# Kernel tuning notes

Measured on AMD Instinct MI355X. Metric: run time of the kernel, lower is better.

The kernel has to match this reference:

```python
import jax, jax.numpy as jnp
import numpy as np

GROUPS = 32
EPS = 1e-6


def group_norm(x, scale, bias):
    b, c, h, w = x.shape
    xg = x.reshape(b, GROUPS, c // GROUPS, h, w)
    mean = xg.mean(axis=(2, 3, 4), keepdims=True)
    var = xg.var(axis=(2, 3, 4), keepdims=True)
    xg = (xg - mean) * jax.lax.rsqrt(var + EPS)
    x = xg.reshape(b, c, h, w)
    return x * scale[None, :, None, None] + bias[None, :, None, None]


def conv1x1(x, w, b):
    # x: [B,C,H,W], w: [O,C], b: [O]
    return jnp.einsum('bchw,oc->bohw', x, w) + b[None, :, None, None]


def setup_inputs() -> dict:
    key = jax.random.key(0)
    ks = jax.random.split(key, 11)
    B, C, H, W = 4, 512, 64, 64
    s = 1.0 / np.sqrt(C)
    return {
        'x': jax.random.normal(ks[0], (B, C, H, W), jnp.float32),
        'gn_scale': jnp.ones((C,), jnp.float32),
        'gn_bias': jnp.zeros((C,), jnp.float32),
        'wq': jax.random.normal(ks[1], (C, C), jnp.float32) * s,
        'bq': jnp.zeros((C,), jnp.float32),
        'wk': jax.random.normal(ks[2], (C, C), jnp.float32) * s,
        'bk': jnp.zeros((C,), jnp.float32),
        'wv': jax.random.normal(ks[3], (C, C), jnp.float32) * s,
        'bv': jnp.zeros((C,), jnp.float32),
        'wp': jax.random.normal(ks[4], (C, C), jnp.float32) * s,
        'bp': jnp.zeros((C,), jnp.float32),
    }


def reference(x, gn_scale, gn_bias, wq, bq, wk, bk, wv, bv, wp, bp):
    b, c, h, w = x.shape
    h_ = group_norm(x, gn_scale, gn_bias)
    q = conv1x1(h_, wq, bq).reshape(b, c, h * w)  # [B,C,N]
    k = conv1x1(h_, wk, bk).reshape(b, c, h * w)
    v = conv1x1(h_, wv, bv).reshape(b, c, h * w)
    # scores[b,i,j] = sum_c q[b,c,i]*k[b,c,j] / sqrt(c)
    scores = jnp.einsum('bci,bcj->bij', q, k) * (c ** -0.5)
    attn = jax.nn.softmax(scores, axis=2)
    # out[b,c,i] = sum_j attn[b,i,j] * v[b,c,j]
    out = jnp.einsum('bij,bcj->bci', attn, v).reshape(b, c, h, w)
    out = conv1x1(out, wp, bp)
    return x + out
```

## Files before the change

kernel.cpp:

```cpp
#include <hip/hip_runtime.h>

#define CDIM 512
#define NDIM 4096
#define BATCH 4

using bf8v = __attribute__((ext_vector_type(8))) __bf16;
using f4v  = __attribute__((ext_vector_type(4))) float;

typedef __attribute__((address_space(1))) unsigned int gu32;
typedef __attribute__((address_space(3))) unsigned int lu32;

static __device__ __forceinline__ unsigned short f2bf(float f) {
  unsigned int u = __float_as_uint(f);
  u += 0x7fffu + ((u >> 16) & 1u);
  return (unsigned short)(u >> 16);
}

static __device__ __forceinline__ bf8v lds_read16(const unsigned short* p) {
  bf8v r;
  unsigned off = (unsigned)(unsigned long long)p;
  asm volatile("ds_read_b128 %0, %1" : "=v"(r) : "v"(off));
  return r;
}

__global__ __launch_bounds__(256) void gn_stats_kernel(
    const float* __restrict__ x, float* __restrict__ stats) {
  const int tid = threadIdx.x;
  const float4* xv = (const float4*)(x + (long)blockIdx.x * 65536);
  float s = 0.f, ss = 0.f;
  for (int i = tid; i < 16384; i += 256) {
    float4 d = xv[i];
    s  += d.x + d.y + d.z + d.w;
    ss += d.x * d.x + d.y * d.y + d.z * d.z + d.w * d.w;
  }
#pragma unroll
  for (int off = 32; off; off >>= 1) {
    s  += __shfl_down(s, off);
    ss += __shfl_down(ss, off);
  }
  __shared__ float red[8];
  if ((tid & 63) == 0) { red[tid >> 6] = s; red[4 + (tid >> 6)] = ss; }
  __syncthreads();
  if (tid == 0) {
    float S  = red[0] + red[1] + red[2] + red[3];
    float SS = red[4] + red[5] + red[6] + red[7];
    float mean = S * (1.f / 65536.f);
    float var  = SS * (1.f / 65536.f) - mean * mean;
    stats[blockIdx.x * 2]     = mean;
    stats[blockIdx.x * 2 + 1] = rsqrtf(var + 1e-6f);
  }
}

__global__ __launch_bounds__(256) void gn_transpose_kernel(
    const float* __restrict__ x, const float* __restrict__ gs,
    const float* __restrict__ gb, const float* __restrict__ stats,
    unsigned short* __restrict__ hT) {
  __shared__ float t[64][65];
  const int tid = threadIdx.x;
  const int b = blockIdx.z;
  const long bbx = (long)b * ((long)CDIM * NDIM);
  const int n0 = blockIdx.x * 64, c0 = blockIdx.y * 64;
  for (int k = 0; k < 4; ++k) {
    int it = tid + k * 256;
    int c = it >> 4, no = (it & 15) << 2;
    int ch = c0 + c;
    int g = ch >> 4;
    float mean = stats[(b * 32 + g) * 2];
    float rstd = stats[(b * 32 + g) * 2 + 1];
    float a  = rstd * gs[ch];
    float bb = gb[ch] - mean * a;
    float4 d = *(const float4*)&x[bbx + (long)ch * NDIM + n0 + no];
    t[no + 0][c] = d.x * a + bb;
    t[no + 1][c] = d.y * a + bb;
    t[no + 2][c] = d.z * a + bb;
    t[no + 3][c] = d.w * a + bb;
  }
  __syncthreads();
  const long bbh = (long)b * ((long)NDIM * CDIM);
  for (int k = 0; k < 2; ++k) {
    int it = tid + k * 256;
    int n = it >> 3, co = (it & 7) << 3;
    unsigned int ow[4];
#pragma unroll
    for (int j = 0; j < 4; ++j) {
      unsigned short lo = f2bf(t[n][co + 2 * j]);
      unsigned short hi = f2bf(t[n][co + 2 * j + 1]);
      ow[j] = (unsigned int)lo | ((unsigned int)hi << 16);
    }
    uint4 o; o.x = ow[0]; o.y = ow[1]; o.z = ow[2]; o.w = ow[3];
    *(uint4*)&hT[bbh + (long)(n0 + n) * CDIM + c0 + co] = o;
  }
}

__global__ __launch_bounds__(256) void prep_kernel(
    const float* __restrict__ wq, const float* __restrict__ wk,
    const float* __restrict__ wv, const float* __restrict__ bq,
    const float* __restrict__ bk, unsigned short* __restrict__ wqkb,
    unsigned short* __restrict__ wvb, float* __restrict__ bqk) {
  int blk = blockIdx.x;
  if (blk < 768) {
    int i = blk * 256 + threadIdx.x;
    const float* src = (blk < 256) ? wq : (blk < 512) ? wk : wv;
    unsigned short* dst = (blk < 256) ? wqkb : (blk < 512) ? (wqkb + 262144) : wvb;
    int j = i - ((blk < 256) ? 0 : (blk < 512) ? 65536 : 131072);
    float4 d = ((const float4*)src)[j];
    ushort4 o;
    o.x = f2bf(d.x); o.y = f2bf(d.y); o.z = f2bf(d.z); o.w = f2bf(d.w);
    ((ushort4*)dst)[j] = o;
  } else {
#pragma unroll
    for (int k = 0; k < 4; ++k) {
      int i = threadIdx.x + k * 256;
      bqk[i] = (i < 512) ? bq[i] : bk[i - 512];
    }
  }
}

__global__ __launch_bounds__(256) void cvt_kernel(
    const float* __restrict__ src, unsigned short* __restrict__ dst, int n4) {
  int i = blockIdx.x * 256 + threadIdx.x;
  if (i >= n4) return;
  float4 d = ((const float4*)src)[i];
  ushort4 o;
  o.x = f2bf(d.x); o.y = f2bf(d.y); o.z = f2bf(d.z); o.w = f2bf(d.w);
  ((ushort4*)dst)[i] = o;
}

template <int BM, int BN, int EPI, int ORD>
__global__ __launch_bounds__(512, 2) void gemm8(
    const unsigned short* __restrict__ A, long sA, int lA,
    const unsigned short* __restrict__ B, long sB, int lB,
    void* __restrict__ Cp, long sC,
    const float* __restrict__ bias,
    const float* __restrict__ X, long sX,
    int GX, int GY, int Nn, int K) {
  constexpr int TM = BM / 32;
  constexpr int TN = BN / 64;
  constexpr int LA = BM / 128;
  constexpr int LB = BN / 128;
  constexpr int VN = 2 * (LA + LB);

  __shared__ __align__(16) unsigned short As[4 * BM * 32];
  __shared__ __align__(16) unsigned short Bs[4 * BN * 32];

  const int tid = threadIdx.x;
  const int nwg = gridDim.x;
  const int g = (blockIdx.x & 7) * (nwg >> 3) + (blockIdx.x >> 3);
  int bx, by, bz;
  if (ORD == 0) { bx = g % GX; int t = g / GX; by = t % GY; bz = t / GY; }
  else          { by = g % GY; int t = g / GY; bx = t % GX; bz = t / GX; }

  A += (long)bz * sA;
  B += (long)bz * sB;
  const int m0 = by * BM;
  const int n0 = bx * BN;
  const int lane = tid & 63;
  const int wv = tid >> 6;
  const int wm = (wv >> 2) * (BM / 2);
  const int wn = (wv & 3) * (BN / 4);
  const int l16 = lane & 15;
  const int quad = lane >> 4;
  const int rdo = ((quad ^ ((l16 >> 1) & 3)) << 3);

  const int rl = tid >> 2;
  const int gl = tid & 3;
  const int swl = ((gl ^ ((rl >> 1) & 3)) << 3);
  const unsigned short* Ag = A + (long)(m0 + rl) * lA + swl;
  const unsigned short* Bg = B + (long)(n0 + rl) * lB + swl;
  unsigned short* Asl = As + wv * 512;
  unsigned short* Bsl = Bs + wv * 512;

  const int nchunk = K >> 5;

  auto stageA = [&](int c) {
    if (c < nchunk) {
#pragma unroll
      for (int i = 0; i < LA; ++i)
        __builtin_amdgcn_global_load_lds(
            (const gu32*)(Ag + (long)i * 128 * lA + c * 32),
            (lu32*)(Asl + (c & 3) * (BM * 32) + i * 4096), 16, 0, 0);
    }
  };
  auto stageB = [&](int c) {
    if (c < nchunk) {
#pragma unroll
      for (int i = 0; i < LB; ++i)
        __builtin_amdgcn_global_load_lds(
            (const gu32*)(Bg + (long)i * 128 * lB + c * 32),
            (lu32*)(Bsl + (c & 3) * (BN * 32) + i * 4096), 16, 0, 0);
    }
  };

  f4v acc[TM][TN] = {};
  f4v accr[TM] = {};
  bf8v ones;
#pragma unroll
  for (int i = 0; i < 8; ++i) ones[i] = (__bf16)1.0f;

  auto body = [&](int d) {
    __builtin_amdgcn_s_barrier();
    stageA(d + 3);
    stageB(d + 3);
    const unsigned short* Ab = As + (d & 3) * (BM * 32);
    const unsigned short* Bb = Bs + (d & 3) * (BN * 32);
    bf8v af[TM], bf[TN];
#pragma unroll
    for (int t = 0; t < TM; ++t)
      af[t] = lds_read16(&Ab[(wm + t * 16 + l16) * 32 + rdo]);
#pragma unroll
    for (int t = 0; t < TN; ++t)
      bf[t] = lds_read16(&Bb[(wn + t * 16 + l16) * 32 + rdo]);
    asm volatile("s_waitcnt lgkmcnt(0)");
    __builtin_amdgcn_sched_barrier(0);
    __builtin_amdgcn_s_setprio(1);
#pragma unroll
    for (int tm = 0; tm < TM; ++tm) {
#pragma unroll
      for (int tn = 0; tn < TN; ++tn)
        acc[tm][tn] = __builtin_amdgcn_mfma_f32_16x16x32_bf16(
            af[tm], bf[tn], acc[tm][tn], 0, 0, 0);
      if (EPI == 3)
        accr[tm] = __builtin_amdgcn_mfma_f32_16x16x32_bf16(
            af[tm], ones, accr[tm], 0, 0, 0);
    }
    __builtin_amdgcn_s_setprio(0);
  };

  stageA(0); stageB(0); stageA(1); stageB(1); stageA(2); stageB(2);

  int d = 0;
  for (; d < nchunk - 2; ++d) {
    if constexpr (VN == 8) asm volatile("s_waitcnt vmcnt(8)");
    else                   asm volatile("s_waitcnt vmcnt(6)");
    body(d);
  }
  if constexpr (VN == 8) asm volatile("s_waitcnt vmcnt(4)");
  else                   asm volatile("s_waitcnt vmcnt(3)");
  body(d); ++d;
  asm volatile("s_waitcnt vmcnt(0)");
  body(d);

  if (EPI == 2) {
#pragma unroll
    for (int tm = 0; tm < TM; ++tm) {
#pragma unroll
      for (int r = 0; r < 4; ++r) {
        const int row = m0 + wm + tm * 16 + quad * 4 + r;
#pragma unroll
        for (int tn = 0; tn < TN; ++tn) {
          const int col = n0 + wn + tn * 16 + l16;
          float e = __expf(acc[tm][tn][r] * 0.044194173824159216f);
          ((unsigned short*)Cp)[(long)bz * sC + (long)row * Nn + col] = f2bf(e);
        }
      }
    }
  } else if (EPI == 3) {
#pragma unroll
    for (int tm = 0; tm < TM; ++tm) {
#pragma unroll
      for (int r = 0; r < 4; ++r) {
        const int row = m0 + wm + tm * 16 + quad * 4 + r;
        const float inv = 1.0f / accr[tm][r];
#pragma unroll
        for (int tn = 0; tn < TN; ++tn) {
          const int col = n0 + wn + tn * 16 + l16;
          ((unsigned short*)Cp)[(long)bz * sC + (long)row * Nn + col] =
              f2bf(acc[tm][tn][r] * inv);
        }
      }
    }
  } else {
#pragma unroll
    for (int tm = 0; tm < TM; ++tm) {
#pragma unroll
      for (int tn = 0; tn < TN; ++tn) {
        const int col = n0 + wn + tn * 16 + l16;
#pragma unroll
        for (int r = 0; r < 4; ++r) {
          const int row = m0 + wm + tm * 16 + quad * 4 + r;
          float val = acc[tm][tn][r];
          if (EPI == 0) {
            val += bias[col];
            ((unsigned short*)Cp)[(long)bz * sC + (long)row * Nn + col] = f2bf(val);
          } else if (EPI == 1) {
            val += bias[row];
            ((unsigned short*)Cp)[(long)bz * sC + (long)row * Nn + col] = f2bf(val);
          } else {
            ((float*)Cp)[(long)bz * sC + (long)row * Nn + col] =
                val + bias[row] + X[(long)bz * sX + (long)row * Nn + col];
          }
        }
      }
    }
  }
}

extern "C" void kernel_launch(void* const* d_in, const int* in_sizes, int n_in,
                              void* d_out, int out_size, void* d_ws, size_t ws_size,
                              hipStream_t stream) {
  (void)in_sizes; (void)n_in; (void)out_size;
  const float* x  = (const float*)d_in[0];
  const float* gs = (const float*)d_in[1];
  const float* gb = (const float*)d_in[2];
  const float* wq = (const float*)d_in[3];
  const float* bq = (const float*)d_in[4];
  const float* wk = (const float*)d_in[5];
  const float* bk = (const float*)d_in[6];
  const float* wv = (const float*)d_in[7];
  const float* bv = (const float*)d_in[8];
  const float* wp = (const float*)d_in[9];
  const float* bp = (const float*)d_in[10];
  float* out = (float*)d_out;

  char* ws = (char*)d_ws;
  const long NC  = (long)NDIM * CDIM;
  const long NQK = (long)NDIM * 1024;
  const long BUF = NC * 2 * BATCH;
  const long NN  = (long)NDIM * NDIM;

  unsigned short* hT   = (unsigned short*)(ws);
  unsigned short* OT   = hT;
  unsigned short* qkT  = (unsigned short*)(ws + BUF);
  unsigned short* vB   = (unsigned short*)(ws + BUF * 3);
  unsigned short* sc   = (unsigned short*)(ws + BUF * 4);
  unsigned short* wqkb = sc;
  unsigned short* wvb  = (unsigned short*)(ws + BUF * 4 + 1048576);
  float* bqk           = (float*)(ws + BUF * 4 + 1572864);
  float* stats         = (float*)(ws + BUF * 4 + 1581056);
  unsigned short* wpb  = qkT;

  gn_stats_kernel<<<BATCH * 32, 256, 0, stream>>>(x, stats);
  gn_transpose_kernel<<<dim3(NDIM / 64, CDIM / 64, BATCH), 256, 0, stream>>>(x, gs, gb, stats, hT);
  prep_kernel<<<769, 256, 0, stream>>>(wq, wk, wv, bq, bk, wqkb, wvb, bqk);

  gemm8<256, 256, 0, 0><<<256, 512, 0, stream>>>(
      hT, NC, CDIM, wqkb, 0, CDIM, qkT, NQK, bqk, nullptr, 0, 4, 16, 1024, CDIM);
  gemm8<128, 256, 1, 1><<<256, 512, 0, stream>>>(
      wvb, 0, CDIM, hT, NC, CDIM, vB, NC, bv, nullptr, 0, 16, 4, NDIM, CDIM);

  if (ws_size >= (size_t)(BUF * 4) + (size_t)(NN * 2) * BATCH) {
    gemm8<256, 256, 2, 0><<<1024, 512, 0, stream>>>(
        qkT, NQK, 1024, qkT + 512, NQK, 1024, sc, NN, nullptr, nullptr, 0,
        16, 16, NDIM, CDIM);
    gemm8<128, 256, 3, 1><<<256, 512, 0, stream>>>(
        sc, NN, NDIM, vB, NC, NDIM, OT, NC, nullptr, nullptr, 0,
        2, 32, CDIM, NDIM);
  } else {
    for (int b = 0; b < BATCH; ++b) {
      gemm8<256, 256, 2, 0><<<256, 512, 0, stream>>>(
          qkT + b * NQK, 0, 1024, qkT + b * NQK + 512, 0, 1024, sc, 0,
          nullptr, nullptr, 0, 16, 16, NDIM, CDIM);
      gemm8<128, 256, 3, 1><<<64, 512, 0, stream>>>(
          sc, 0, NDIM, vB + b * NC, 0, NDIM, OT + b * NC, 0,
          nullptr, nullptr, 0, 2, 32, CDIM, NDIM);
    }
  }

  cvt_kernel<<<256, 256, 0, stream>>>(wp, wpb, 65536);
  gemm8<128, 256, 4, 1><<<256, 512, 0, stream>>>(
      wpb, 0, CDIM, OT, NC, CDIM, out, NC, bp, x, NC, 16, 4, NDIM, CDIM);
}
```

Before: 358.5 us.

## Double-buffer LDS fragment reads to overlap with MFMA in GEMM main loop

Restructures the GEMM K-loop so the LDS fragment reads for the next chunk are issued before the MFMAs of the current chunk run, using two register fragment sets (A/B ping-pong) and a loop unrolled by two. The aim is to hide LDS read latency behind matrix math instead of waiting on lgkmcnt before each chunk's MFMAs. It also merges the A/B staging lambdas and retunes the vmcnt waits. In exchange it doubles the fragment registers, which may pressure occupancy under launch_bounds(512,2). The pipeline tail assumes an even chunk count.

```diff
diff --git a/kernel.cpp b/kernel.cpp
--- a/kernel.cpp
+++ b/kernel.cpp
@@ -138,7 +138,7 @@
   constexpr int TN = BN / 64;
   constexpr int LA = BM / 128;
   constexpr int LB = BN / 128;
-  constexpr int VN = 2 * (LA + LB);
+  constexpr int L  = LA + LB;
 
   __shared__ __align__(16) unsigned short As[4 * BM * 32];
   __shared__ __align__(16) unsigned short Bs[4 * BN * 32];
@@ -172,17 +172,13 @@
 
   const int nchunk = K >> 5;
 
-  auto stageA = [&](int c) {
+  auto stage = [&](int c) {
     if (c < nchunk) {
 #pragma unroll
       for (int i = 0; i < LA; ++i)
         __builtin_amdgcn_global_load_lds(
             (const gu32*)(Ag + (long)i * 128 * lA + c * 32),
             (lu32*)(Asl + (c & 3) * (BM * 32) + i * 4096), 16, 0, 0);
-    }
-  };
-  auto stageB = [&](int c) {
-    if (c < nchunk) {
 #pragma unroll
       for (int i = 0; i < LB; ++i)
         __builtin_amdgcn_global_load_lds(
@@ -197,21 +193,20 @@
 #pragma unroll
   for (int i = 0; i < 8; ++i) ones[i] = (__bf16)1.0f;
 
-  auto body = [&](int d) {
-    __builtin_amdgcn_s_barrier();
-    stageA(d + 3);
-    stageB(d + 3);
-    const unsigned short* Ab = As + (d & 3) * (BM * 32);
-    const unsigned short* Bb = Bs + (d & 3) * (BN * 32);
-    bf8v af[TM], bf[TN];
+  bf8v afA[TM], bfA[TN], afB[TM], bfB[TN];
+
+  auto readfr = [&](int c, bf8v* af, bf8v* bf) {
+    const unsigned short* Ab = As + (c & 3) * (BM * 32);
+    const unsigned short* Bb = Bs + (c & 3) * (BN * 32);
 #pragma unroll
     for (int t = 0; t < TM; ++t)
       af[t] = lds_read16(&Ab[(wm + t * 16 + l16) * 32 + rdo]);
 #pragma unroll
     for (int t = 0; t < TN; ++t)
       bf[t] = lds_read16(&Bb[(wn + t * 16 + l16) * 32 + rdo]);
-    asm volatile("s_waitcnt lgkmcnt(0)");
-    __builtin_amdgcn_sched_barrier(0);
+  };
+
+  auto mfma = [&](const bf8v* af, const bf8v* bf) {
     __builtin_amdgcn_s_setprio(1);
 #pragma unroll
     for (int tm = 0; tm < TM; ++tm) {
@@ -226,19 +221,37 @@
     __builtin_amdgcn_s_setprio(0);
   };
 
-  stageA(0); stageB(0); stageA(1); stageB(1); stageA(2); stageB(2);
+  auto seg = [&](int d, const bf8v* afC, const bf8v* bfC,
+                 bf8v* afN, bf8v* bfN) {
+    __builtin_amdgcn_s_barrier();
+    stage(d + 3);
+    asm volatile("s_waitcnt lgkmcnt(0)");
+    __builtin_amdgcn_sched_barrier(0);
+    readfr(d + 1, afN, bfN);
+    __builtin_amdgcn_sched_barrier(0);
+    mfma(afC, bfC);
+  };
+
+  stage(0); stage(1); stage(2);
+  if constexpr (L == 4) asm volatile("s_waitcnt vmcnt(8)");
+  else                  asm volatile("s_waitcnt vmcnt(6)");
+  __builtin_amdgcn_s_barrier();
+  readfr(0, afA, bfA);
 
   int d = 0;
-  for (; d < nchunk - 2; ++d) {
-    if constexpr (VN == 8) asm volatile("s_waitcnt vmcnt(8)");
-    else                   asm volatile("s_waitcnt vmcnt(6)");
-    body(d);
-  }
-  if constexpr (VN == 8) asm volatile("s_waitcnt vmcnt(4)");
-  else                   asm volatile("s_waitcnt vmcnt(3)");
-  body(d); ++d;
+  for (; d < nchunk - 2; d += 2) {
+    if constexpr (L == 4) asm volatile("s_waitcnt vmcnt(4)");
+    else                  asm volatile("s_waitcnt vmcnt(3)");
+    seg(d, afA, bfA, afB, bfB);
+    if constexpr (L == 4) asm volatile("s_waitcnt vmcnt(4)");
+    else                  asm volatile("s_waitcnt vmcnt(3)");
+    seg(d + 1, afB, bfB, afA, bfA);
+  }
   asm volatile("s_waitcnt vmcnt(0)");
-  body(d);
+  seg(d, afA, bfA, afB, bfB);
+  asm volatile("s_waitcnt lgkmcnt(0)");
+  __builtin_amdgcn_sched_barrier(0);
+  mfma(afB, bfB);
 
   if (EPI == 2) {
 #pragma unroll
```

New measurement: 363.0 us. Within noise of the previous version (+1.3%).

## Switch GEMM mainloop to K=64 double-buffered tiles with interleaved LDS reads and MFMA

Applied to the files above, without the earlier changes.

Restructures the bf16 GEMM mainloop from a 4-stage ring of K=32 chunks to a 2-stage double buffer of K=64 tiles with a new XOR swizzle. Within each tile, A-fragment LDS reads are split into clusters and issued ahead of the MFMA groups, with partial lgkmcnt waits, so LDS latency overlaps compute. This halves the number of barriers per K. The cost is shallower global prefetch: each iteration now does a full vmcnt(0) wait, which may expose global-load latency.

```diff
diff --git a/kernel.cpp b/kernel.cpp
--- a/kernel.cpp
+++ b/kernel.cpp
@@ -136,12 +136,11 @@
     int GX, int GY, int Nn, int K) {
   constexpr int TM = BM / 32;
   constexpr int TN = BN / 64;
-  constexpr int LA = BM / 128;
-  constexpr int LB = BN / 128;
-  constexpr int VN = 2 * (LA + LB);
-
-  __shared__ __align__(16) unsigned short As[4 * BM * 32];
-  __shared__ __align__(16) unsigned short Bs[4 * BN * 32];
+  constexpr int LA = BM / 64;
+  constexpr int LB = BN / 64;
+
+  __shared__ __align__(16) unsigned short As[2 * BM * 64];
+  __shared__ __align__(16) unsigned short Bs[2 * BN * 64];
 
   const int tid = threadIdx.x;
   const int nwg = gridDim.x;
@@ -160,34 +159,32 @@
   const int wn = (wv & 3) * (BN / 4);
   const int l16 = lane & 15;
   const int quad = lane >> 4;
-  const int rdo = ((quad ^ ((l16 >> 1) & 3)) << 3);
-
-  const int rl = tid >> 2;
-  const int gl = tid & 3;
-  const int swl = ((gl ^ ((rl >> 1) & 3)) << 3);
-  const unsigned short* Ag = A + (long)(m0 + rl) * lA + swl;
-  const unsigned short* Bg = B + (long)(n0 + rl) * lB + swl;
-  unsigned short* Asl = As + wv * 512;
-  unsigned short* Bsl = Bs + wv * 512;
-
-  const int nchunk = K >> 5;
-
-  auto stageA = [&](int c) {
-    if (c < nchunk) {
+  const int sw7 = l16 & 7;
+  const int rg0 = ((0 + quad) ^ sw7) << 3;
+  const int rg1 = ((4 + quad) ^ sw7) << 3;
+
+  const int r0s  = wv * 8 + (lane >> 3);
+  const int gsrc = ((lane & 7) ^ (lane >> 3)) << 3;
+  const unsigned short* Ag = A + (long)(m0 + r0s) * lA + gsrc;
+  const unsigned short* Bg = B + (long)(n0 + r0s) * lB + gsrc;
+
+  const int nt = K >> 6;
+
+  auto stage = [&](int t) {
+    if (t < nt) {
+      const int k0 = t << 6;
+      unsigned short* Ad = As + (t & 1) * (BM * 64) + wv * 512;
+      unsigned short* Bd = Bs + (t & 1) * (BN * 64) + wv * 512;
 #pragma unroll
       for (int i = 0; i < LA; ++i)
         __builtin_amdgcn_global_load_lds(
-            (const gu32*)(Ag + (long)i * 128 * lA + c * 32),
-            (lu32*)(Asl + (c & 3) * (BM * 32) + i * 4096), 16, 0, 0);
-    }
-  };
-  auto stageB = [&](int c) {
-    if (c < nchunk) {
+            (const gu32*)(Ag + (long)i * 64 * lA + k0),
+            (lu32*)(Ad + i * 4096), 16, 0, 0);
 #pragma unroll
       for (int i = 0; i < LB; ++i)
         __builtin_amdgcn_global_load_lds(
-            (const gu32*)(Bg + (long)i * 128 * lB + c * 32),
-            (lu32*)(Bsl + (c & 3) * (BN * 32) + i * 4096), 16, 0, 0);
+            (const gu32*)(Bg + (long)i * 64 * lB + k0),
+            (lu32*)(Bd + i * 4096), 16, 0, 0);
     }
   };
 
@@ -197,48 +194,79 @@
 #pragma unroll
   for (int i = 0; i < 8; ++i) ones[i] = (__bf16)1.0f;
 
-  auto body = [&](int d) {
-    __builtin_amdgcn_s_barrier();
-    stageA(d + 3);
-    stageB(d + 3);
-    const unsigned short* Ab = As + (d & 3) * (BM * 32);
-    const unsigned short* Bb = Bs + (d & 3) * (BN * 32);
-    bf8v af[TM], bf[TN];
-#pragma unroll
-    for (int t = 0; t < TM; ++t)
-      af[t] = lds_read16(&Ab[(wm + t * 16 + l16) * 32 + rdo]);
-#pragma unroll
-    for (int t = 0; t < TN; ++t)
-      bf[t] = lds_read16(&Bb[(wn + t * 16 + l16) * 32 + rdo]);
-    asm volatile("s_waitcnt lgkmcnt(0)");
-    __builtin_amdgcn_sched_barrier(0);
+  bf8v bfr[TN][2];
+  bf8v afA[2][2], afB[2][2];
+
+  const unsigned short* Ab;
+  const unsigned short* Bb;
+
+  auto rdB = [&]() {
+#pragma unroll
+    for (int tn = 0; tn < TN; ++tn) {
+      bfr[tn][0] = lds_read16(&Bb[(wn + tn * 16 + l16) * 64 + rg0]);
+      bfr[tn][1] = lds_read16(&Bb[(wn + tn * 16 + l16) * 64 + rg1]);
+    }
+  };
+  auto rdA = [&](int q, bf8v (&fr)[2][2]) {
+#pragma unroll
+    for (int dr = 0; dr < 2; ++dr) {
+      fr[dr][0] = lds_read16(&Ab[(wm + (q * 2 + dr) * 16 + l16) * 64 + rg0]);
+      fr[dr][1] = lds_read16(&Ab[(wm + (q * 2 + dr) * 16 + l16) * 64 + rg1]);
+    }
+  };
+  auto clus = [&](int q, bf8v (&fr)[2][2]) {
     __builtin_amdgcn_s_setprio(1);
 #pragma unroll
-    for (int tm = 0; tm < TM; ++tm) {
-#pragma unroll
-      for (int tn = 0; tn < TN; ++tn)
-        acc[tm][tn] = __builtin_amdgcn_mfma_f32_16x16x32_bf16(
-            af[tm], bf[tn], acc[tm][tn], 0, 0, 0);
-      if (EPI == 3)
-        accr[tm] = __builtin_amdgcn_mfma_f32_16x16x32_bf16(
-            af[tm], ones, accr[tm], 0, 0, 0);
-    }
+    for (int kk = 0; kk < 2; ++kk)
+#pragma unroll
+      for (int dr = 0; dr < 2; ++dr) {
+        const int tm = q * 2 + dr;
+#pragma unroll
+        for (int tn = 0; tn < TN; ++tn)
+          acc[tm][tn] = __builtin_amdgcn_mfma_f32_16x16x32_bf16(
+              fr[dr][kk], bfr[tn][kk], acc[tm][tn], 0, 0, 0);
+        if (EPI == 3)
+          accr[tm] = __builtin_amdgcn_mfma_f32_16x16x32_bf16(
+              fr[dr][kk], ones, accr[tm], 0, 0, 0);
+      }
     __builtin_amdgcn_s_setprio(0);
   };
 
-  stageA(0); stageB(0); stageA(1); stageB(1); stageA(2); stageB(2);
-
-  int d = 0;
-  for (; d < nchunk - 2; ++d) {
-    if constexpr (VN == 8) asm volatile("s_waitcnt vmcnt(8)");
-    else                   asm volatile("s_waitcnt vmcnt(6)");
-    body(d);
-  }
-  if constexpr (VN == 8) asm volatile("s_waitcnt vmcnt(4)");
-  else                   asm volatile("s_waitcnt vmcnt(3)");
-  body(d); ++d;
-  asm volatile("s_waitcnt vmcnt(0)");
-  body(d);
+  stage(0);
+  for (int t = 0; t < nt; ++t) {
+    asm volatile("s_waitcnt vmcnt(0)");
+    __builtin_amdgcn_s_barrier();
+    stage(t + 1);
+    Ab = As + (t & 1) * (BM * 64);
+    Bb = Bs + (t & 1) * (BN * 64);
+    rdB();
+    rdA(0, afA);
+    if constexpr (TM == 8) {
+      rdA(1, afB);
+      asm volatile("s_waitcnt lgkmcnt(4)");
+      __builtin_amdgcn_sched_barrier(0);
+      clus(0, afA);
+      rdA(2, afA);
+      asm volatile("s_waitcnt lgkmcnt(4)");
+      __builtin_amdgcn_sched_barrier(0);
+      clus(1, afB);
+      rdA(3, afB);
+      asm volatile("s_waitcnt lgkmcnt(4)");
+      __builtin_amdgcn_sched_barrier(0);
+      clus(2, afA);
+      asm volatile("s_waitcnt lgkmcnt(0)");
+      __builtin_amdgcn_sched_barrier(0);
+      clus(3, afB);
+    } else {
+      rdA(1, afB);
+      asm volatile("s_waitcnt lgkmcnt(4)");
+      __builtin_amdgcn_sched_barrier(0);
+      clus(0, afA);
+      asm volatile("s_waitcnt lgkmcnt(0)");
+      __builtin_amdgcn_sched_barrier(0);
+      clus(1, afB);
+    }
+  }
 
   if (EPI == 2) {
 #pragma unroll
```

Result: no change. 354.1 us (-1.2%).
